# Kernel tuning notes

Hardware: AMD Instinct MI355X
Metric: run time of the kernel (lower is better)

The kernel has to match this reference:

```python
import jax, jax.numpy as jnp
import numpy as np

DIM = 4096
N_HEADS = 32
N_KV_HEADS = 8
HEAD_DIM = DIM // N_HEADS  # 128
B, S = 2, 2048
LN_EPS = 1e-5


def _precompute_freqs_cis(seqlen, head_dim, theta=10000.0):
    inv = 1.0 / (theta ** (np.arange(0, head_dim, 2, dtype=np.float32) / head_dim))  # [HD/2]
    ang = np.outer(np.arange(seqlen, dtype=np.float32), inv)  # [S, HD/2]
    return jnp.asarray(np.stack([np.cos(ang), np.sin(ang)], axis=-1))  # [S, HD/2, 2]


def setup_inputs() -> dict:
    key = jax.random.key(0)
    ks = jax.random.split(key, 9)
    std = 0.02
    return {
        "x": jax.random.normal(ks[0], (B, S, DIM), dtype=jnp.float32),
        "freqs_cis": _precompute_freqs_cis(S, HEAD_DIM),
        "wq": jax.random.normal(ks[1], (N_HEADS * HEAD_DIM, DIM), dtype=jnp.float32) * std,
        "wk": jax.random.normal(ks[2], (N_KV_HEADS * HEAD_DIM, DIM), dtype=jnp.float32) * std,
        "wv": jax.random.normal(ks[3], (N_KV_HEADS * HEAD_DIM, DIM), dtype=jnp.float32) * std,
        "wo": jax.random.normal(ks[4], (DIM, N_HEADS * HEAD_DIM), dtype=jnp.float32) * std,
        "q_norm_w": jnp.ones((N_HEADS * HEAD_DIM,), dtype=jnp.float32),
        "q_norm_b": jnp.zeros((N_HEADS * HEAD_DIM,), dtype=jnp.float32),
        "k_norm_w": jnp.ones((N_KV_HEADS * HEAD_DIM,), dtype=jnp.float32),
        "k_norm_b": jnp.zeros((N_KV_HEADS * HEAD_DIM,), dtype=jnp.float32),
    }


def _layernorm(v, w, b):
    mu = jnp.mean(v, axis=-1, keepdims=True)
    var = jnp.var(v, axis=-1, keepdims=True)
    return (v - mu) * jax.lax.rsqrt(var + LN_EPS) * w + b


def _rope(t, fc):
    # t: [B, S, nh, HD]; fc: [S, HD/2, 2] = (cos, sin)
    b_, s_, nh, hd = t.shape
    tr = t.reshape(b_, s_, nh, hd // 2, 2)
    a, bb = tr[..., 0], tr[..., 1]
    cos = fc[None, :, None, :, 0]
    sin = fc[None, :, None, :, 1]
    out = jnp.stack([a * cos - bb * sin, a * sin + bb * cos], axis=-1)
    return out.reshape(t.shape)


def reference(x, freqs_cis, wq, wk, wv, wo, q_norm_w, q_norm_b, k_norm_w, k_norm_b):
    bsz, seqlen, _ = x.shape
    H, KV, HD = N_HEADS, N_KV_HEADS, HEAD_DIM
    R = H // KV  # GQA repeat factor

    xq = jnp.einsum('bsd,ed->bse', x, wq)
    xk = jnp.einsum('bsd,ed->bse', x, wk)
    xv = jnp.einsum('bsd,ed->bse', x, wv)

    xq = _layernorm(xq, q_norm_w, q_norm_b)
    xk = _layernorm(xk, k_norm_w, k_norm_b)

    xq = xq.reshape(bsz, seqlen, H, HD)
    xk = xk.reshape(bsz, seqlen, KV, HD)
    xv = xv.reshape(bsz, seqlen, KV, HD)

    xq = _rope(xq, freqs_cis)
    xk = _rope(xk, freqs_cis)

    # GQA: group q heads as (kv, rep) and broadcast k/v instead of materializing repeats
    xqg = xq.reshape(bsz, seqlen, KV, R, HD)
    scale = 1.0 / jnp.sqrt(jnp.float32(HD))
    scores = jnp.einsum('bqkrh,bskh->bkrqs', xqg, xk) * scale  # [B,KV,R,S,S]
    attn = jax.nn.softmax(scores, axis=-1)
    out = jnp.einsum('bkrqs,bskh->bqkrh', attn, xv).reshape(bsz, seqlen, H * HD)
    return jnp.einsum('bse,de->bsd', out, wo)
```

## Files before the change

kernel.cpp:

```cpp
#include <hip/hip_runtime.h>
#include <cstdint>

typedef _Float16 half4v __attribute__((ext_vector_type(4)));
typedef _Float16 half8v __attribute__((ext_vector_type(8)));
typedef __fp16   fp16x2 __attribute__((ext_vector_type(2)));
typedef float    f32x4v __attribute__((ext_vector_type(4)));

#define DIM    4096
#define SEQ    2048
#define NBATCH 2
#define NHEAD  32
#define NKVH   8
#define HDIM   128
#define MROWS  (NBATCH*SEQ)
#define QKV_N  6144
#define KOFF   4096
#define VOFF   5120

__device__ __forceinline__ void gl_lds16(const void* g, void* l) {
  __builtin_amdgcn_global_load_lds(
      (const __attribute__((address_space(1))) void*)g,
      (__attribute__((address_space(3))) void*)l, 16, 0, 0);
}

__global__ __launch_bounds__(256) void cvt_kernel(const float* __restrict__ in,
                                                  _Float16* __restrict__ out, int n8) {
  int stride = gridDim.x * blockDim.x;
  for (int i = blockIdx.x * blockDim.x + threadIdx.x; i < n8; i += stride) {
    const float4* p = (const float4*)(in + (size_t)i * 8);
    float4 a = p[0], b = p[1];
    half8v h;
    h[0] = (_Float16)a.x; h[1] = (_Float16)a.y; h[2] = (_Float16)a.z; h[3] = (_Float16)a.w;
    h[4] = (_Float16)b.x; h[5] = (_Float16)b.y; h[6] = (_Float16)b.z; h[7] = (_Float16)b.w;
    *(half8v*)(out + (size_t)i * 8) = h;
  }
}

#define SBAR() do { asm volatile("" ::: "memory"); \
                    __builtin_amdgcn_s_barrier();  \
                    asm volatile("" ::: "memory"); } while (0)
#define LGK0() asm volatile("s_waitcnt lgkmcnt(0)" ::: "memory")
#define VM6()  asm volatile("s_waitcnt vmcnt(6)" ::: "memory")
#define VM4()  asm volatile("s_waitcnt vmcnt(4)" ::: "memory")
#define VM0()  asm volatile("s_waitcnt vmcnt(0)" ::: "memory")

#define STAGE_HALF(Gm, rowbase, kidx, h, buf) do {                                   \
    gl_lds16((Gm) + (size_t)((rowbase) + (h)*128 + srow) * K + (kidx)*64 + sslot8,   \
             (buf) + (h)*8192 + w*512);                                              \
    gl_lds16((Gm) + (size_t)((rowbase) + (h)*128 + 64 + srow) * K + (kidx)*64 + sslot8, \
             (buf) + (h)*8192 + 4096 + w*512);                                       \
  } while (0)

#define MFMA_Q(hm, hn, bf)                                                   \
    _Pragma("unroll") for (int kk = 0; kk < 2; ++kk)                         \
      _Pragma("unroll") for (int mi = 0; mi < 4; ++mi)                       \
        _Pragma("unroll") for (int ni = 0; ni < 2; ++ni)                     \
          acc[(hm) * 4 + mi][(hn) * 2 + ni] =                                \
              __builtin_amdgcn_mfma_f32_16x16x32_f16(                        \
                  a[mi][kk], bf[ni][kk], acc[(hm) * 4 + mi][(hn) * 2 + ni], 0, 0, 0)

#define KSTEP(kcur, AC, BC, AN)                                              \
  do {                                                                       \
    const int k_ = (kcur);                                                   \
    half8v a[4][2], b0[2][2], b1[2][2];                                      \
                                         \
    _Pragma("unroll") for (int mi = 0; mi < 4; ++mi)                         \
      _Pragma("unroll") for (int kk = 0; kk < 2; ++kk)                       \
        a[mi][kk] = *(const half8v*)((AC) + (wm * 128 + mi * 16 + li) * 64 + \
                                     (((kk * 4 + g) ^ li7) * 8));            \
    _Pragma("unroll") for (int ni = 0; ni < 2; ++ni)                         \
      _Pragma("unroll") for (int kk = 0; kk < 2; ++kk)                       \
        b0[ni][kk] = *(const half8v*)((BC) + (wn * 64 + ni * 16 + li) * 64 + \
                                      (((kk * 4 + g) ^ li7) * 8));           \
    if (k_ + 1 < nkt) STAGE_HALF(A, bm, k_ + 1, 1, (AN));                    \
    SBAR(); LGK0();                                                          \
    __builtin_amdgcn_s_setprio(1);                                           \
    MFMA_Q(0, 0, b0);                                                        \
    __builtin_amdgcn_s_setprio(0);                                           \
    SBAR();                                                                  \
                                         \
    _Pragma("unroll") for (int ni = 0; ni < 2; ++ni)                         \
      _Pragma("unroll") for (int kk = 0; kk < 2; ++kk)                       \
        b1[ni][kk] = *(const half8v*)((BC) + (wn * 64 + 32 + ni * 16 + li) * 64 + \
                                      (((kk * 4 + g) ^ li7) * 8));           \
    SBAR(); LGK0();                                                          \
    __builtin_amdgcn_s_setprio(1);                                           \
    MFMA_Q(0, 1, b1);                                                        \
    __builtin_amdgcn_s_setprio(0);                                           \
    SBAR();                                                                  \
          \
    _Pragma("unroll") for (int mi = 0; mi < 4; ++mi)                         \
      _Pragma("unroll") for (int kk = 0; kk < 2; ++kk)                       \
        a[mi][kk] = *(const half8v*)((AC) + (wm * 128 + 64 + mi * 16 + li) * 64 + \
                                     (((kk * 4 + g) ^ li7) * 8));            \
    if (k_ + 2 < nkt) {                                                      \
      STAGE_HALF(B, bn, k_ + 2, 0, (BC));                                    \
      STAGE_HALF(B, bn, k_ + 2, 1, (BC));                                    \
    }                                                                        \
    SBAR(); LGK0();                                                          \
    __builtin_amdgcn_s_setprio(1);                                           \
    MFMA_Q(1, 1, b1);                                                        \
    __builtin_amdgcn_s_setprio(0);                                           \
    SBAR();                                                                  \
          \
    if (k_ + 2 < nkt) STAGE_HALF(A, bm, k_ + 2, 0, (AC));                    \
    SBAR();                                                                  \
    __builtin_amdgcn_s_setprio(1);                                           \
    MFMA_Q(1, 0, b0);                                                        \
    __builtin_amdgcn_s_setprio(0);                                           \
    if (k_ + 2 < nkt) { VM6(); } else if (k_ + 1 < nkt) { VM0(); }           \
    SBAR();                                                                  \
  } while (0)

template<int OUTF16>
__global__ __launch_bounds__(512, 2) void gemm256(const _Float16* __restrict__ A,
                                                  const _Float16* __restrict__ B,
                                                  void* __restrict__ Cp,
                                                  int N, int K, int nbx) {
  __shared__ __align__(16) _Float16 As[2][256 * 64];
  __shared__ __align__(16) _Float16 Bs[2][256 * 64];
  const int tid = threadIdx.x, lane = tid & 63, w = tid >> 6;
  const int g = lane >> 4, li = lane & 15, li7 = lane & 7;
  const int wm = w >> 2, wn = w & 3;
  const int nwg = gridDim.x, orig = blockIdx.x;
  const int wgid = (nwg & 7) ? orig : ((orig & 7) * (nwg >> 3) + (orig >> 3));
  const int bm = (wgid / nbx) * 256, bn = (wgid % nbx) * 256;
  const int srow = tid >> 3;
  const int sslot8 = ((lane & 7) ^ ((lane >> 3) & 7)) * 8;
  const int nkt = K >> 6;
  _Float16* As0 = &As[0][0]; _Float16* As1 = &As[1][0];
  _Float16* Bs0 = &Bs[0][0]; _Float16* Bs1 = &Bs[1][0];

  f32x4v acc[8][4] = {};

  STAGE_HALF(A, bm, 0, 0, As0);
  STAGE_HALF(A, bm, 0, 1, As0);
  STAGE_HALF(B, bn, 0, 0, Bs0);
  STAGE_HALF(B, bn, 0, 1, Bs0);
  if (nkt > 1) {
    STAGE_HALF(B, bn, 1, 0, Bs1);
    STAGE_HALF(B, bn, 1, 1, Bs1);
    STAGE_HALF(A, bm, 1, 0, As1);
    VM6();
  } else {
    VM0();
  }
  SBAR();

  for (int k = 0; k < nkt; k += 2) {
    KSTEP(k,     As0, Bs0, As1);
    KSTEP(k + 1, As1, Bs1, As0);
  }

  const int r0 = bm + wm * 128 + g * 4;
  const int c0 = bn + wn * 64 + li;
#pragma unroll
  for (int mi = 0; mi < 8; ++mi)
#pragma unroll
    for (int ni = 0; ni < 4; ++ni)
#pragma unroll
      for (int j = 0; j < 4; ++j) {
        size_t idx = (size_t)(r0 + mi * 16 + j) * N + (c0 + ni * 16);
        if (OUTF16) ((_Float16*)Cp)[idx] = (_Float16)acc[mi][ni][j];
        else        ((float*)Cp)[idx]    = acc[mi][ni][j];
      }
}

template<int E>
__global__ __launch_bounds__(256) void ln_rope(_Float16* __restrict__ t, int ldt,
                                               const float* __restrict__ gw,
                                               const float* __restrict__ gb,
                                               const float* __restrict__ fc) {
  constexpr int EPT = E / 256;
  const int row = blockIdx.x;
  const int s = row & (SEQ - 1);
  const int tid = threadIdx.x, lane = tid & 63, w = tid >> 6;
  _Float16* rp = t + (size_t)row * ldt + tid * EPT;
  float v[EPT];
#pragma unroll
  for (int i = 0; i < EPT; i += 4) {
    half4v hv = *(const half4v*)(rp + i);
    v[i] = (float)hv[0]; v[i+1] = (float)hv[1]; v[i+2] = (float)hv[2]; v[i+3] = (float)hv[3];
  }
  float sum = 0.f, ssq = 0.f;
#pragma unroll
  for (int i = 0; i < EPT; ++i) { sum += v[i]; ssq += v[i] * v[i]; }
#pragma unroll
  for (int off = 1; off < 64; off <<= 1) { sum += __shfl_xor(sum, off); ssq += __shfl_xor(ssq, off); }
  __shared__ float red[8];
  if (lane == 0) { red[w] = sum; red[4 + w] = ssq; }
  __syncthreads();
  sum = red[0] + red[1] + red[2] + red[3];
  ssq = red[4] + red[5] + red[6] + red[7];
  const float mu = sum * (1.0f / E);
  const float rstd = rsqrtf(ssq * (1.0f / E) - mu * mu + 1e-5f);
  float ov[EPT];
#pragma unroll
  for (int i = 0; i < EPT; i += 2) {
    int e = tid * EPT + i;
    int hd = e & (HDIM - 1);
    float2 cs = *(const float2*)(fc + (size_t)s * HDIM + (hd >> 1) * 2);
    float a = (v[i]   - mu) * rstd * gw[e]   + gb[e];
    float b = (v[i+1] - mu) * rstd * gw[e+1] + gb[e+1];
    ov[i]   = a * cs.x - b * cs.y;
    ov[i+1] = a * cs.y + b * cs.x;
  }
#pragma unroll
  for (int i = 0; i < EPT; i += 4) {
    half4v hv;
    hv[0] = (_Float16)ov[i];   hv[1] = (_Float16)ov[i+1];
    hv[2] = (_Float16)ov[i+2]; hv[3] = (_Float16)ov[i+3];
    *(half4v*)(rp + i) = hv;
  }
}

__global__ __launch_bounds__(256) void vtrans(const _Float16* __restrict__ qkv,
                                              _Float16* __restrict__ vt) {
  __shared__ _Float16 tile[64][136];
  const int blk = blockIdx.x;
  const int st = blk & 31, kvh = (blk >> 5) & 7, b = blk >> 8;
  const int t = threadIdx.x;
  const _Float16* src = qkv + (size_t)(b * SEQ + st * 64) * QKV_N + VOFF + kvh * 128;
#pragma unroll
  for (int i = 0; i < 4; ++i) {
    int sl = (t >> 4) + i * 16;
    int h0 = (t & 15) * 8;
    *(half8v*)&tile[sl][h0] = *(const half8v*)(src + (size_t)sl * QKV_N + h0);
  }
  __syncthreads();
  const int hd = t & 127, half = t >> 7;
  _Float16* dst = vt + ((size_t)((b * NKVH + kvh) * 128 + hd)) * SEQ + st * 64 + half * 32;
#pragma unroll
  for (int j = 0; j < 32; j += 8) {
    half8v v;
#pragma unroll
    for (int e = 0; e < 8; ++e) v[e] = tile[half * 32 + j + e][hd];
    *(half8v*)(dst + j) = v;
  }
}

__global__ __launch_bounds__(256, 2) void attn_kernel(const _Float16* __restrict__ QKV,
                                                      const _Float16* __restrict__ VT,
                                                      _Float16* __restrict__ Oa) {
  __shared__ __align__(16) _Float16 Ksh[2][64 * 128];
  __shared__ __align__(16) char Vsh[128 * 128];
  const int tid = threadIdx.x, lane = tid & 63, w = tid >> 6;
  const int g = lane >> 4, li = lane & 15;
  const int blk = blockIdx.x;
  const int qt = blk & 15, h = (blk >> 4) & 31, b = blk >> 9;
  const int kvh = h >> 2;
  const size_t LD = QKV_N;
  const _Float16* Qb = QKV + (size_t)(b * SEQ) * LD + h * HDIM;
  const _Float16* Kb = QKV + (size_t)(b * SEQ) * LD + KOFF + kvh * HDIM;
  const _Float16* VTb = VT + (size_t)((b * NKVH + kvh) * 128) * SEQ;
  const int lg = lane >> 4;
  const int gbit = (lane >> 5) & 1;

  half8v qf[2][4];
#pragma unroll
  for (int s = 0; s < 2; ++s) {
    const int qrow = qt * 128 + w * 32 + s * 16 + li;
#pragma unroll
    for (int kk = 0; kk < 4; ++kk) {
      half8v q0 = *(const half8v*)(Qb + (size_t)qrow * LD + kk * 32 + g * 8);
#pragma unroll
      for (int e = 0; e < 8; ++e) q0[e] = q0[e] * (_Float16)0.08838834764831845f;
      qf[s][kk] = q0;
    }
  }
  float mrow[2] = {-1e30f, -1e30f}, lrow[2] = {0.f, 0.f};
  f32x4v oacc[2][8] = {};

#define ASTAGE_K(kt_, buf_) do {                                              \
    _Pragma("unroll") for (int i_ = 0; i_ < 4; ++i_) {                        \
      int chunk = i_ * 4 + w;                                                 \
      int r = chunk * 4 + lg;                                                 \
      int sc8 = ((lane & 15) ^ (r & 7)) * 8;                                  \
      gl_lds16(Kb + (size_t)((kt_) * 64 + r) * LD + sc8, (buf_) + chunk * 512); \
    } } while (0)

#define ASTAGE_V(kt_, buf_) do {                                              \
    _Pragma("unroll") for (int i_ = 0; i_ < 4; ++i_) {                        \
      int chunk = i_ * 4 + w;                                                 \
      int hd_ = chunk * 8 + (lane >> 3);                                      \
      int keyh = (chunk ^ (lane >> 3)) & 7;                                   \
      int p_ = lane & 7;                                                      \
      gl_lds16(VTb + (size_t)hd_ * SEQ + (kt_) * 64 + ((p_ ^ keyh) * 8),      \
               (buf_) + chunk * 1024);                                        \
    } } while (0)

  ASTAGE_K(0, Ksh[0]);
  ASTAGE_V(0, Vsh);
  VM0();
  SBAR();

  const int NT = SEQ / 64;
  for (int kt = 0; kt < NT; ++kt) {
    const int cur = kt & 1;
    const _Float16* Kcur = Ksh[cur];
    f32x4v sc0[4] = {}, sc1[4] = {};
    __builtin_amdgcn_s_setprio(1);
#pragma unroll
    for (int kk = 0; kk < 4; ++kk) {
#pragma unroll
      for (int ni = 0; ni < 4; ++ni) {
        half8v kf = *(const half8v*)(Kcur + (16 * ni + li) * 128 + ((4 * kk + g) ^ (li & 7)) * 8);
        sc0[ni] = __builtin_amdgcn_mfma_f32_16x16x32_f16(kf, qf[0][kk], sc0[ni], 0, 0, 0);
        sc1[ni] = __builtin_amdgcn_mfma_f32_16x16x32_f16(kf, qf[1][kk], sc1[ni], 0, 0, 0);
      }
    }
    __builtin_amdgcn_s_setprio(0);
    if (kt + 1 < NT) ASTAGE_K(kt + 1, Ksh[cur ^ 1]);
    uint32_t u[2][4][2];
#pragma unroll
    for (int s = 0; s < 2; ++s) {
      f32x4v* sc = s ? sc1 : sc0;
      float m16 = sc[0][0];
#pragma unroll
      for (int ni = 0; ni < 4; ++ni)
        m16 = fmaxf(m16, fmaxf(fmaxf(sc[ni][0], sc[ni][1]), fmaxf(sc[ni][2], sc[ni][3])));
      m16 = fmaxf(m16, __shfl_xor(m16, 16));
      m16 = fmaxf(m16, __shfl_xor(m16, 32));
      if (!__all(m16 - mrow[s] <= 8.0f)) {
        const float mn = fmaxf(mrow[s], m16);
        const float sfo = __expf(mrow[s] - mn);
        mrow[s] = mn;
        lrow[s] *= sfo;
        float sfj[4];
#pragma unroll
        for (int j = 0; j < 4; ++j) sfj[j] = __shfl(sfo, (lane & 48) | (4 * g + j));
#pragma unroll
        for (int nio = 0; nio < 8; ++nio) {
          oacc[s][nio][0] *= sfj[0]; oacc[s][nio][1] *= sfj[1];
          oacc[s][nio][2] *= sfj[2]; oacc[s][nio][3] *= sfj[3];
        }
      }
      float rs = 0.f;
#pragma unroll
      for (int ni = 0; ni < 4; ++ni)
#pragma unroll
        for (int j = 0; j < 4; ++j) { float pv = __expf(sc[ni][j] - mrow[s]); sc[ni][j] = pv; rs += pv; }
      rs += __shfl_xor(rs, 16); rs += __shfl_xor(rs, 32);
      lrow[s] += rs;
#pragma unroll
      for (int ni = 0; ni < 4; ++ni) {
        fp16x2 p0 = __builtin_amdgcn_cvt_pkrtz(sc[ni][0], sc[ni][1]);
        fp16x2 p1 = __builtin_amdgcn_cvt_pkrtz(sc[ni][2], sc[ni][3]);
        u[s][ni][0] = *(uint32_t*)&p0;
        u[s][ni][1] = *(uint32_t*)&p1;
      }
    }
    if (kt + 1 < NT) { VM4(); } else { VM0(); }
    SBAR();
#pragma unroll
    for (int kk = 0; kk < 2; ++kk) {
      half8v pa[2];
#pragma unroll
      for (int s = 0; s < 2; ++s) {
        uint32_t own0 = gbit ? u[s][2*kk+1][0] : u[s][2*kk][0];
        uint32_t own1 = gbit ? u[s][2*kk+1][1] : u[s][2*kk][1];
        uint32_t oth0 = gbit ? u[s][2*kk][0]   : u[s][2*kk+1][0];
        uint32_t oth1 = gbit ? u[s][2*kk][1]   : u[s][2*kk+1][1];
        uint32_t r16_0 = (uint32_t)__shfl_xor((int)own0, 16);
        uint32_t r16_1 = (uint32_t)__shfl_xor((int)own1, 16);
        uint32_t r32_0 = (uint32_t)__shfl_xor((int)oth0, 32);
        uint32_t r32_1 = (uint32_t)__shfl_xor((int)oth1, 32);
        uint32_t r48_0 = (uint32_t)__shfl_xor((int)oth0, 48);
        uint32_t r48_1 = (uint32_t)__shfl_xor((int)oth1, 48);
        uint32_t d0 = (g == 0) ? own0 : (g == 1) ? r48_0 : (g == 2) ? r32_0 : r16_0;
        uint32_t d1 = (g == 0) ? own1 : (g == 1) ? r48_1 : (g == 2) ? r32_1 : r16_1;
        uint32_t d2 = (g == 0) ? r16_0 : (g == 1) ? r32_0 : (g == 2) ? r48_0 : own0;
        uint32_t d3 = (g == 0) ? r16_1 : (g == 1) ? r32_1 : (g == 2) ? r48_1 : own1;
        union { uint32_t u4[4]; half8v hh; } pu;
        pu.u4[0] = d0; pu.u4[1] = d1; pu.u4[2] = d2; pu.u4[3] = d3;
        pa[s] = pu.hh;
      }
      __builtin_amdgcn_s_setprio(1);
#pragma unroll
      for (int nio = 0; nio < 8; ++nio) {
        int r = nio * 16 + li;
        int key = ((r >> 3) ^ r) & 7;
        half8v bv = *(const half8v*)(Vsh + r * 128 + (((kk * 4 + g) ^ key) << 4));
        oacc[0][nio] = __builtin_amdgcn_mfma_f32_16x16x32_f16(pa[0], bv, oacc[0][nio], 0, 0, 0);
        oacc[1][nio] = __builtin_amdgcn_mfma_f32_16x16x32_f16(pa[1], bv, oacc[1][nio], 0, 0, 0);
      }
      __builtin_amdgcn_s_setprio(0);
    }
    VM0();
    SBAR();
    if (kt + 1 < NT) ASTAGE_V(kt + 1, Vsh);
  }
#undef ASTAGE_K
#undef ASTAGE_V
#pragma unroll
  for (int s = 0; s < 2; ++s) {
    float rinv[4];
#pragma unroll
    for (int j = 0; j < 4; ++j)
      rinv[j] = 1.0f / __shfl(lrow[s], (lane & 48) | (4 * g + j));
    _Float16* Ob = Oa + (size_t)(b * SEQ + qt * 128 + w * 32 + s * 16) * DIM + h * HDIM;
#pragma unroll
    for (int j = 0; j < 4; ++j)
#pragma unroll
      for (int nio = 0; nio < 8; ++nio)
        Ob[(size_t)(4 * g + j) * DIM + nio * 16 + li] = (_Float16)(oacc[s][nio][j] * rinv[j]);
  }
}

extern "C" void kernel_launch(void* const* d_in, const int* in_sizes, int n_in,
                              void* d_out, int out_size, void* d_ws, size_t ws_size,
                              hipStream_t stream) {
  const float* x   = (const float*)d_in[0];
  const float* fc  = (const float*)d_in[1];
  const float* wq  = (const float*)d_in[2];
  const float* wk  = (const float*)d_in[3];
  const float* wv  = (const float*)d_in[4];
  const float* wo  = (const float*)d_in[5];
  const float* qnw = (const float*)d_in[6];
  const float* qnb = (const float*)d_in[7];
  const float* knw = (const float*)d_in[8];
  const float* knb = (const float*)d_in[9];
  float* out = (float*)d_out;
  (void)in_sizes; (void)n_in; (void)out_size;

  const size_t MB = 1024 * 1024;
  if (ws_size < 128 * MB) return;
  char* ws = (char*)d_ws;
  _Float16* x_h    = (_Float16*)(ws + 0);
  _Float16* wqkv_h = (_Float16*)(ws + 32 * MB);
  _Float16* wk_h   = (_Float16*)(ws + 64 * MB);
  _Float16* wv_h   = (_Float16*)(ws + 72 * MB);
  _Float16* qkv_h  = (_Float16*)(ws + 80 * MB);
  _Float16* wo_h   = wqkv_h;
  _Float16* vt_h   = wk_h;
  _Float16* ao_h   = x_h;

  cvt_kernel<<<2048, 256, 0, stream>>>(x,  x_h,    (MROWS * DIM) / 8);
  cvt_kernel<<<2048, 256, 0, stream>>>(wq, wqkv_h, (DIM * DIM) / 8);
  cvt_kernel<<<1024, 256, 0, stream>>>(wk, wk_h,   (1024 * DIM) / 8);
  cvt_kernel<<<1024, 256, 0, stream>>>(wv, wv_h,   (1024 * DIM) / 8);

  gemm256<1><<<(MROWS / 256) * (QKV_N / 256), 512, 0, stream>>>(x_h, wqkv_h, qkv_h,
                                                                QKV_N, DIM, QKV_N / 256);

  cvt_kernel<<<2048, 256, 0, stream>>>(wo, wo_h, (DIM * DIM) / 8);

  vtrans<<<NBATCH * NKVH * (SEQ / 64), 256, 0, stream>>>(qkv_h, vt_h);

  ln_rope<4096><<<MROWS, 256, 0, stream>>>(qkv_h,        QKV_N, qnw, qnb, fc);
  ln_rope<1024><<<MROWS, 256, 0, stream>>>(qkv_h + KOFF, QKV_N, knw, knb, fc);

  attn_kernel<<<NBATCH * NHEAD * (SEQ / 128), 256, 0, stream>>>(qkv_h, vt_h, ao_h);

  gemm256<0><<<(MROWS / 256) * (DIM / 256), 512, 0, stream>>>(ao_h, wo_h, out,
                                                              DIM, DIM, DIM / 256);
}
```

Measured before the change: 649.8 us.

## Fuse QKV GEMM into a persistent 256-block kernel with balanced tile split

Replaces the 384-workgroup QKV GEMM launch with a 256-workgroup kernel. Each workgroup computes one full 256x256 Q tile and then one 256x128 half-tile of the K/V columns, using a new half-width K-step macro. The aim is to remove the partial second wave on the machine's CUs (256 = one wave at 2 per CU) by balancing work per workgroup. It adds a second, narrower GEMM phase with its own prologue and lower MFMA density per LDS load.

```diff
diff --git a/kernel.cpp b/kernel.cpp
--- a/kernel.cpp
+++ b/kernel.cpp
@@ -109,6 +109,50 @@
     MFMA_Q(1, 0, b0);                                                        \
     __builtin_amdgcn_s_setprio(0);                                           \
     if (k_ + 2 < nkt) { VM6(); } else if (k_ + 1 < nkt) { VM0(); }           \
+    SBAR();                                                                  \
+  } while (0)
+
+#define HKSTEP(kcur, AC, BC, AN)                                             \
+  do {                                                                       \
+    const int k_ = (kcur);                                                   \
+    half8v a[4][2], bb[2][2];                                                \
+                                                     \
+    _Pragma("unroll") for (int mi = 0; mi < 4; ++mi)                         \
+      _Pragma("unroll") for (int kk = 0; kk < 2; ++kk)                       \
+        a[mi][kk] = *(const half8v*)((AC) + (wm * 128 + mi * 16 + li) * 64 + \
+                                     (((kk * 4 + g) ^ li7) * 8));            \
+    _Pragma("unroll") for (int ni = 0; ni < 2; ++ni)                         \
+      _Pragma("unroll") for (int kk = 0; kk < 2; ++kk)                       \
+        bb[ni][kk] = *(const half8v*)((BC) + (wn * 32 + ni * 16 + li) * 64 + \
+                                      (((kk * 4 + g) ^ li7) * 8));           \
+    if (k_ + 1 < nkt) STAGE_HALF(A, bm2, k_ + 1, 1, (AN));                   \
+    SBAR(); LGK0();                                                          \
+    __builtin_amdgcn_s_setprio(1);                                           \
+    _Pragma("unroll") for (int kk = 0; kk < 2; ++kk)                         \
+      _Pragma("unroll") for (int mi = 0; mi < 4; ++mi)                       \
+        _Pragma("unroll") for (int ni = 0; ni < 2; ++ni)                     \
+          acc2[mi][ni] = __builtin_amdgcn_mfma_f32_16x16x32_f16(             \
+              a[mi][kk], bb[ni][kk], acc2[mi][ni], 0, 0, 0);                 \
+    __builtin_amdgcn_s_setprio(0);                                           \
+    SBAR();                                                                  \
+                            \
+    _Pragma("unroll") for (int mi = 0; mi < 4; ++mi)                         \
+      _Pragma("unroll") for (int kk = 0; kk < 2; ++kk)                       \
+        a[mi][kk] = *(const half8v*)((AC) + (wm * 128 + 64 + mi * 16 + li) * 64 + \
+                                     (((kk * 4 + g) ^ li7) * 8));            \
+    if (k_ + 2 < nkt) {                                                      \
+      STAGE_HALF(B, bn2, k_ + 2, 0, (BC));                                   \
+      STAGE_HALF(A, bm2, k_ + 2, 0, (AC));                                   \
+    }                                                                        \
+    SBAR(); LGK0();                                                          \
+    __builtin_amdgcn_s_setprio(1);                                           \
+    _Pragma("unroll") for (int kk = 0; kk < 2; ++kk)                         \
+      _Pragma("unroll") for (int mi = 0; mi < 4; ++mi)                       \
+        _Pragma("unroll") for (int ni = 0; ni < 2; ++ni)                     \
+          acc2[4 + mi][ni] = __builtin_amdgcn_mfma_f32_16x16x32_f16(         \
+              a[mi][kk], bb[ni][kk], acc2[4 + mi][ni], 0, 0, 0);             \
+    __builtin_amdgcn_s_setprio(0);                                           \
+    if (k_ + 2 < nkt) { VM4(); } else if (k_ + 1 < nkt) { VM0(); }           \
     SBAR();                                                                  \
   } while (0)
 
@@ -164,6 +208,77 @@
         if (OUTF16) ((_Float16*)Cp)[idx] = (_Float16)acc[mi][ni][j];
         else        ((float*)Cp)[idx]    = acc[mi][ni][j];
       }
+}
+
+__global__ __launch_bounds__(512, 2) void gemm_qkv(const _Float16* __restrict__ A,
+                                                   const _Float16* __restrict__ B,
+                                                   _Float16* __restrict__ Cp) {
+  __shared__ __align__(16) _Float16 As[2][256 * 64];
+  __shared__ __align__(16) _Float16 Bs[2][256 * 64];
+  const int tid = threadIdx.x, lane = tid & 63, w = tid >> 6;
+  const int g = lane >> 4, li = lane & 15, li7 = lane & 7;
+  const int wm = w >> 2, wn = w & 3;
+  const int K = DIM, N = QKV_N, nkt = DIM >> 6;
+  const int orig = blockIdx.x;
+  const int wgid = (orig & 7) * 32 + (orig >> 3);
+  const int bm = (wgid >> 4) * 256, bn = (wgid & 15) * 256;
+  const int t2 = wgid >> 1;
+  const int bm2 = (t2 >> 3) * 256;
+  const int bn2 = (16 + (t2 & 7)) * 256 + (wgid & 1) * 128;
+  const int srow = tid >> 3;
+  const int sslot8 = ((lane & 7) ^ ((lane >> 3) & 7)) * 8;
+  _Float16* As0 = &As[0][0]; _Float16* As1 = &As[1][0];
+  _Float16* Bs0 = &Bs[0][0]; _Float16* Bs1 = &Bs[1][0];
+
+  {
+    f32x4v acc[8][4] = {};
+    STAGE_HALF(A, bm, 0, 0, As0);
+    STAGE_HALF(A, bm, 0, 1, As0);
+    STAGE_HALF(B, bn, 0, 0, Bs0);
+    STAGE_HALF(B, bn, 0, 1, Bs0);
+    STAGE_HALF(B, bn, 1, 0, Bs1);
+    STAGE_HALF(B, bn, 1, 1, Bs1);
+    STAGE_HALF(A, bm, 1, 0, As1);
+    VM6();
+    SBAR();
+    for (int k = 0; k < nkt; k += 2) {
+      KSTEP(k,     As0, Bs0, As1);
+      KSTEP(k + 1, As1, Bs1, As0);
+    }
+    const int r0 = bm + wm * 128 + g * 4;
+    const int c0 = bn + wn * 64 + li;
+#pragma unroll
+    for (int mi = 0; mi < 8; ++mi)
+#pragma unroll
+      for (int ni = 0; ni < 4; ++ni)
+#pragma unroll
+        for (int j = 0; j < 4; ++j)
+          Cp[(size_t)(r0 + mi * 16 + j) * N + (c0 + ni * 16)] = (_Float16)acc[mi][ni][j];
+  }
+
+  {
+    f32x4v acc2[8][2] = {};
+    STAGE_HALF(A, bm2, 0, 0, As0);
+    STAGE_HALF(A, bm2, 0, 1, As0);
+    STAGE_HALF(B, bn2, 0, 0, Bs0);
+    STAGE_HALF(B, bn2, 1, 0, Bs1);
+    STAGE_HALF(A, bm2, 1, 0, As1);
+    VM4();
+    SBAR();
+    for (int k = 0; k < nkt; k += 2) {
+      HKSTEP(k,     As0, Bs0, As1);
+      HKSTEP(k + 1, As1, Bs1, As0);
+    }
+    const int r0 = bm2 + wm * 128 + g * 4;
+    const int c0 = bn2 + wn * 32 + li;
+#pragma unroll
+    for (int mi = 0; mi < 8; ++mi)
+#pragma unroll
+      for (int ni = 0; ni < 2; ++ni)
+#pragma unroll
+        for (int j = 0; j < 4; ++j)
+          Cp[(size_t)(r0 + mi * 16 + j) * N + (c0 + ni * 16)] = (_Float16)acc2[mi][ni][j];
+  }
 }
 
 template<int E>
@@ -440,8 +555,7 @@
   cvt_kernel<<<1024, 256, 0, stream>>>(wk, wk_h,   (1024 * DIM) / 8);
   cvt_kernel<<<1024, 256, 0, stream>>>(wv, wv_h,   (1024 * DIM) / 8);
 
-  gemm256<1><<<(MROWS / 256) * (QKV_N / 256), 512, 0, stream>>>(x_h, wqkv_h, qkv_h,
-                                                                QKV_N, DIM, QKV_N / 256);
+  gemm_qkv<<<256, 512, 0, stream>>>(x_h, wqkv_h, qkv_h);
 
   cvt_kernel<<<2048, 256, 0, stream>>>(wo, wo_h, (DIM * DIM) / 8);
 
```

After: 618.0 us. 4.9% less time.
